# Kernel optimization log

Measured on AMD Instinct MI355X. Metric: run time of the kernel, lower is better.

The kernel has to match this reference:

```python
import jax, jax.numpy as jnp
import numpy as np

S, B, I = 512, 64, 1024
H = 1024 // 2  # per-direction hidden (MyBiGRU halves hidden_size)


def _gru(x, h0, Wx, Wh, b):
    """Single-direction GRU, faithful to MyGRU.forward.
    x: (S,B,I); h0: (B,H); Wx: (3,I,H) gates [r,u,h]; Wh: (3,H,H); b: (3,H).
    Note: candidate uses (reset_gate * state) @ Whh, matching torch operator
    precedence in `reset_gate * state @ self.weight_hh`.
    """
    # Precompute all input projections once: (S, 3, B, H)
    xg = jnp.einsum('sbi,gih->sgbh', x, Wx)

    def step(h, xt):
        r = jax.nn.sigmoid(xt[0] + h @ Wh[0] + b[0])
        u = jax.nn.sigmoid(xt[1] + h @ Wh[1] + b[1])
        c = jnp.tanh(xt[2] + (r * h) @ Wh[2] + b[2])
        h_new = u * h + (1.0 - u) * c
        return h_new, h_new

    h_last, hs = jax.lax.scan(step, h0, xg)
    return hs, h_last  # (S,B,H), (B,H)


def setup_inputs() -> dict:
    key = jax.random.key(0)
    ks = jax.random.split(key, 6)
    std = jnp.float32(0.01)
    return {
        "x": jax.random.normal(ks[0], (S, B, I), jnp.float32),
        "initial_state": jax.random.normal(ks[1], (B, 2 * H), jnp.float32),
        "Wx_f": std * jax.random.normal(ks[2], (3, I, H), jnp.float32),
        "Wh_f": std * jax.random.normal(ks[3], (3, H, H), jnp.float32),
        "b_f": jnp.zeros((3, H), jnp.float32),
        "Wx_b": std * jax.random.normal(ks[4], (3, I, H), jnp.float32),
        "Wh_b": std * jax.random.normal(ks[5], (3, H, H), jnp.float32),
        "b_b": jnp.zeros((3, H), jnp.float32),
    }


def reference(x, initial_state, Wx_f, Wh_f, b_f, Wx_b, Wh_b, b_b):
    h0_f = initial_state[:, :H]
    h0_b = initial_state[:, H:]
    fwd_out, fwd_state = _gru(x, h0_f, Wx_f, Wh_f, b_f)
    bwd_out, bwd_state = _gru(x[::-1], h0_b, Wx_b, Wh_b, b_b)
    outputs = jnp.concatenate([fwd_out, bwd_out[::-1]], axis=-1)  # (S,B,2H)
    state = jnp.concatenate([fwd_state, bwd_state], axis=-1)      # (B,2H)
    return outputs, state
```

## Files before the change

kernel.cpp:

```cpp
#include <hip/hip_runtime.h>
#include <hip/hip_bf16.h>


typedef __attribute__((ext_vector_type(8))) short short8;
typedef __attribute__((ext_vector_type(4))) float f32x4;

#define SENT 0x7FC0
#define SENT64 0x7FC07FC07FC07FC0ULL

__device__ __forceinline__ unsigned short f2bf(float f) {
    unsigned u = __builtin_bit_cast(unsigned, f);
    u += 0x7FFFu + ((u >> 16) & 1u);
    return (unsigned short)(u >> 16);
}
__device__ __forceinline__ float bf2f(unsigned short h) {
    unsigned u = ((unsigned)h) << 16;
    return __builtin_bit_cast(float, u);
}
__device__ __forceinline__ float xv(unsigned long long p, int jj) {
    return bf2f((unsigned short)(p >> (16 * jj)));
}
__device__ __forceinline__ int imin(int a, int b) { return a < b ? a : b; }


__global__ __launch_bounds__(256) void k_cvt_x(const float* __restrict__ x,
                                               unsigned short* __restrict__ xb) {
    size_t gid = (size_t)blockIdx.x * 256 + threadIdx.x;
    f32x4 a = ((const f32x4*)x)[gid * 2];
    f32x4 b = ((const f32x4*)x)[gid * 2 + 1];
    short8 o;
    o[0] = (short)f2bf(a[0]); o[1] = (short)f2bf(a[1]);
    o[2] = (short)f2bf(a[2]); o[3] = (short)f2bf(a[3]);
    o[4] = (short)f2bf(b[0]); o[5] = (short)f2bf(b[1]);
    o[6] = (short)f2bf(b[2]); o[7] = (short)f2bf(b[3]);
    ((short8*)xb)[gid] = o;
}

__global__ __launch_bounds__(256) void k_cvt_w(const float* __restrict__ Wxf,
                                               const float* __restrict__ Wxb,
                                               unsigned short* __restrict__ wt) {
    int gid = blockIdx.x * 256 + threadIdx.x;
    int n = gid >> 7, kc = gid & 127;
    const float* src = (n < 1536) ? Wxf : Wxb;
    int nn = (n >= 1536) ? n - 1536 : n;
    int g = nn >> 9, h = nn & 511;
    short8 o;
#pragma unroll
    for (int j = 0; j < 8; ++j)
        o[j] = (short)f2bf(src[(size_t)(g * 1024 + kc * 8 + j) * 512 + h]);
    *(short8*)(wt + (size_t)n * 1024 + kc * 8) = o;
}

__global__ __launch_bounds__(256) void k_cvt_whsl(const float* __restrict__ Whf,
                                                  const float* __restrict__ Whb,
                                                  unsigned short* __restrict__ o) {
    int gid = blockIdx.x * 256 + threadIdx.x;
    int kc = gid & 63;
    int r = gid >> 6;
    int c = r & 15; r >>= 4;
    int g = r % 3;  r /= 3;
    int w = r & 31, d = r >> 5;
    const float* src = d ? Whb : Whf;
    short8 v;
#pragma unroll
    for (int j = 0; j < 8; ++j)
        v[j] = (short)f2bf(src[(size_t)(g * 512 + kc * 8 + j) * 512 + w * 16 + c]);
    *(short8*)(o + ((size_t)((d * 32 + w) * 3 + g) * 16 + c) * 512 + kc * 8) = v;
}

__global__ __launch_bounds__(256) void k_sent(unsigned short* __restrict__ h4,
                                              unsigned short* __restrict__ rh4) {
    int gid = blockIdx.x * 256 + threadIdx.x;
    short8 s;
#pragma unroll
    for (int j = 0; j < 8; ++j) s[j] = (short)SENT;
    ((short8*)h4)[gid] = s;
    ((short8*)rh4)[gid] = s;
}

__global__ __launch_bounds__(256) void k_init(const float* __restrict__ h0,
                                              unsigned short* __restrict__ h4) {
    int gid = blockIdx.x * 256 + threadIdx.x;
    int b = gid >> 10, ch = gid & 1023;
    int d = ch >> 9, k = ch & 511;
    h4[((size_t)d * 64 + b) * 512 + k] = f2bf(h0[gid]);
}


__global__ __launch_bounds__(256) void k_gemm(const unsigned short* __restrict__ A,
                                              const unsigned short* __restrict__ Bt,
                                              unsigned short* __restrict__ C) {
    __shared__ unsigned short Al[128 * 40];
    __shared__ unsigned short Bl[128 * 40];
    const int n0 = blockIdx.x * 128;
    const int m0 = blockIdx.y * 128;
    const int t = threadIdx.x, wave = t >> 6, lane = t & 63;
    const int lg = lane >> 4, lr = lane & 15;
    const int wm = wave >> 1, wn = wave & 1;
    const int lrow = t >> 2, lkb = t & 3;

    f32x4 acc[4][4] = {};
    for (int kt = 0; kt < 32; ++kt) {
        const int k0 = kt * 32;
#pragma unroll
        for (int p = 0; p < 2; ++p) {
            int row = lrow + p * 64;
            *(short8*)(Al + row * 40 + lkb * 8) =
                *(const short8*)(A + (size_t)(m0 + row) * 1024 + k0 + lkb * 8);
            *(short8*)(Bl + row * 40 + lkb * 8) =
                *(const short8*)(Bt + (size_t)(n0 + row) * 1024 + k0 + lkb * 8);
        }
        __syncthreads();
        short8 af[4], bfr[4];
#pragma unroll
        for (int mi = 0; mi < 4; ++mi)
            af[mi] = *(const short8*)(Al + (wm * 64 + mi * 16 + lr) * 40 + lg * 8);
#pragma unroll
        for (int ni = 0; ni < 4; ++ni)
            bfr[ni] = *(const short8*)(Bl + (wn * 64 + ni * 16 + lr) * 40 + lg * 8);
#pragma unroll
        for (int mi = 0; mi < 4; ++mi)
#pragma unroll
            for (int ni = 0; ni < 4; ++ni)
                acc[mi][ni] = __builtin_amdgcn_mfma_f32_16x16x32_bf16(af[mi], bfr[ni],
                                                                      acc[mi][ni], 0, 0, 0);
        __syncthreads();
    }
#pragma unroll
    for (int mi = 0; mi < 4; ++mi)
#pragma unroll
        for (int ni = 0; ni < 4; ++ni) {
            int m = m0 + wm * 64 + mi * 16 + lg * 4;
            int n = n0 + wn * 64 + ni * 16 + lr;
            int dd = n >= 1536;
            int nn = n - dd * 1536;
            int g = nn >> 9, h = nn & 511;
            size_t colbase = (size_t)dd * 98304 + (size_t)(h >> 4) * 3072 +
                             (size_t)((h >> 2) & 3) * 12 + g * 4 + (h & 3);
#pragma unroll
            for (int jj = 0; jj < 4; ++jj) {
                int mm = m + jj;
                int s = mm >> 6, brow = mm & 63;
                C[(size_t)s * 196608 + colbase + (size_t)brow * 48] = f2bf(acc[mi][ni][jj]);
            }
        }
}


__device__ __forceinline__ void wait_frag(const char* p, short8* fr) {
    for (;;) {
        asm volatile(
            "global_load_dwordx4 %0, %16, off sc1\n\t"
            "global_load_dwordx4 %1, %16, off offset:64 sc1\n\t"
            "global_load_dwordx4 %2, %16, off offset:128 sc1\n\t"
            "global_load_dwordx4 %3, %16, off offset:192 sc1\n\t"
            "global_load_dwordx4 %4, %16, off offset:256 sc1\n\t"
            "global_load_dwordx4 %5, %16, off offset:320 sc1\n\t"
            "global_load_dwordx4 %6, %16, off offset:384 sc1\n\t"
            "global_load_dwordx4 %7, %16, off offset:448 sc1\n\t"
            "global_load_dwordx4 %8, %16, off offset:512 sc1\n\t"
            "global_load_dwordx4 %9, %16, off offset:576 sc1\n\t"
            "global_load_dwordx4 %10, %16, off offset:640 sc1\n\t"
            "global_load_dwordx4 %11, %16, off offset:704 sc1\n\t"
            "global_load_dwordx4 %12, %16, off offset:768 sc1\n\t"
            "global_load_dwordx4 %13, %16, off offset:832 sc1\n\t"
            "global_load_dwordx4 %14, %16, off offset:896 sc1\n\t"
            "global_load_dwordx4 %15, %16, off offset:960 sc1"
            : "=v"(fr[0]), "=v"(fr[1]), "=v"(fr[2]), "=v"(fr[3]),
              "=v"(fr[4]), "=v"(fr[5]), "=v"(fr[6]), "=v"(fr[7]),
              "=v"(fr[8]), "=v"(fr[9]), "=v"(fr[10]), "=v"(fr[11]),
              "=v"(fr[12]), "=v"(fr[13]), "=v"(fr[14]), "=v"(fr[15])
            : "v"(p) : "memory");
        asm volatile("s_waitcnt vmcnt(0)" ::: "memory");
        int bad = 0;
#pragma unroll
        for (int i = 0; i < 16; ++i)
            bad |= (((unsigned short)fr[i][0]) == SENT) |
                   (((unsigned short)fr[i][4]) == SENT);
        if (!__any(bad)) break;
        __builtin_amdgcn_s_sleep(2);
    }
    __builtin_amdgcn_sched_barrier(0);
}


__global__ __launch_bounds__(320) void k_rec(const unsigned short* __restrict__ xgr,
                                             const unsigned short* __restrict__ whsl,
                                             const float* __restrict__ h0,
                                             const float* __restrict__ b_f,
                                             const float* __restrict__ b_b,
                                             unsigned long long* h4,
                                             unsigned long long* rh4,
                                             float* __restrict__ out) {
    __shared__ char Wlb[98304];
    __shared__ char xls[24576];
    __shared__ int xg_ready;
    __shared__ int xg_ack[4];

    const int w = blockIdx.x;
    const int t = threadIdx.x;
    const int wave5 = t >> 6, lane = t & 63;

    if (t == 0) {
        xg_ready = 0;
        xg_ack[0] = xg_ack[1] = xg_ack[2] = xg_ack[3] = 0;
    }
    for (int i = 0; i < 20; ++i) {
        int c = t + i * 320;
        if (c < 6144) {
            int half = (c >= 3072);
            int byte = (c - half * 3072) << 4;
            int swz = byte ^ (((byte >> 10) & 7) << 4);
            *(short8*)(Wlb + half * 49152 + swz) =
                *(const short8*)((const char*)whsl + (size_t)(half * 32 + w) * 49152 + byte);
        }
    }
    __syncthreads();

    if (wave5 == 4) {
        for (int it = 0; it < 512; ++it) {
            if (it >= 2) {
                for (;;) {
                    int a0 = __hip_atomic_load(&xg_ack[0], __ATOMIC_RELAXED, __HIP_MEMORY_SCOPE_WORKGROUP);
                    int a1 = __hip_atomic_load(&xg_ack[1], __ATOMIC_RELAXED, __HIP_MEMORY_SCOPE_WORKGROUP);
                    int a2 = __hip_atomic_load(&xg_ack[2], __ATOMIC_RELAXED, __HIP_MEMORY_SCOPE_WORKGROUP);
                    int a3 = __hip_atomic_load(&xg_ack[3], __ATOMIC_RELAXED, __HIP_MEMORY_SCOPE_WORKGROUP);
                    if (imin(imin(a0, a1), imin(a2, a3)) >= it - 1) break;
                    __builtin_amdgcn_s_sleep(1);
                }
            }
            const char* pf = (const char*)xgr + (size_t)it * 393216 +
                             (size_t)w * 6144 + lane * 96;
            const char* pb = (const char*)xgr + (size_t)(511 - it) * 393216 + 196608 +
                             (size_t)w * 6144 + lane * 96;
            short8 vf[6], vb[6];
#pragma unroll
            for (int k = 0; k < 6; ++k) {
                vf[k] = *(const short8*)(pf + k * 16);
                vb[k] = *(const short8*)(pb + k * 16);
            }
            char* dst = xls + (it & 1) * 12288 + lane * 96;
#pragma unroll
            for (int k = 0; k < 6; ++k) {
                *(short8*)(dst + k * 16) = vf[k];
                *(short8*)(dst + 6144 + k * 16) = vb[k];
            }
            __builtin_amdgcn_fence(__ATOMIC_RELEASE, "workgroup");
            if (lane == 0)
                __hip_atomic_store(&xg_ready, it + 1, __ATOMIC_RELAXED, __HIP_MEMORY_SCOPE_WORKGROUP);
        }
        return;
    }

    const int wave = wave5, lg = lane >> 4, lr = lane & 15;
    const int b = wave * 16 + lr;
    const int cc = w * 16 + lg * 4;
    const int cswz = (lr & 7) << 4;

    const f32x4 bRf = *(const f32x4*)(b_f + cc);
    const f32x4 bUf = *(const f32x4*)(b_f + 512 + cc);
    const f32x4 bCf = *(const f32x4*)(b_f + 1024 + cc);
    const f32x4 bRb = *(const f32x4*)(b_b + cc);
    const f32x4 bUb = *(const f32x4*)(b_b + 512 + cc);
    const f32x4 bCb = *(const f32x4*)(b_b + 1024 + cc);

    float hf[4], hbo[4];
#pragma unroll
    for (int jj = 0; jj < 4; ++jj) {
        hf[jj]  = h0[(size_t)b * 1024 + cc + jj];
        hbo[jj] = h0[(size_t)b * 1024 + 512 + cc + jj];
    }

    const size_t rof = (size_t)b * 1024;
    const size_t rob = (size_t)(64 + b) * 1024;
    const int fro  = lg * 16;
    const int pubo = w * 32 + lg * 8;
    const int xoff = (b * 4 + lg) * 24;
    char* hbP = (char*)h4;
    char* rbP = (char*)rh4;

    for (int it = 0; it < 512; ++it) {
        const size_t slot  = (size_t)(it & 3) << 17;
        const size_t nslot = (size_t)((it + 1) & 3) << 17;
        const size_t oslot = (size_t)((it + 3) & 3) << 17;

        short8 fr[16];
        wait_frag(hbP + slot + rof + fro, fr);
        __hip_atomic_store((unsigned long long*)(hbP + oslot + rof + pubo), SENT64,
                           __ATOMIC_RELAXED, __HIP_MEMORY_SCOPE_AGENT);

        while (__hip_atomic_load(&xg_ready, __ATOMIC_RELAXED, __HIP_MEMORY_SCOPE_WORKGROUP) < it + 1)
            __builtin_amdgcn_s_sleep(1);
        __builtin_amdgcn_fence(__ATOMIC_ACQUIRE, "workgroup");
        const char* xp = xls + (it & 1) * 12288 + xoff;
        const unsigned long long xfR = *(const unsigned long long*)(xp);
        const unsigned long long xfU = *(const unsigned long long*)(xp + 8);
        const unsigned long long xfC = *(const unsigned long long*)(xp + 16);
        const unsigned long long xbR = *(const unsigned long long*)(xp + 6144);
        const unsigned long long xbU = *(const unsigned long long*)(xp + 6144 + 8);
        const unsigned long long xbC = *(const unsigned long long*)(xp + 6144 + 16);

        f32x4 aR = {0.f, 0.f, 0.f, 0.f}, aU = {0.f, 0.f, 0.f, 0.f};
#pragma unroll
        for (int ks = 0; ks < 16; ++ks) {
            int koff = ks * 64 + lg * 16;
            short8 w0 = *(const short8*)(Wlb + (((lr << 10) + koff) ^ cswz));
            short8 w1 = *(const short8*)(Wlb + ((16384 + (lr << 10) + koff) ^ cswz));
            aR = __builtin_amdgcn_mfma_f32_16x16x32_bf16(w0, fr[ks], aR, 0, 0, 0);
            aU = __builtin_amdgcn_mfma_f32_16x16x32_bf16(w1, fr[ks], aU, 0, 0, 0);
        }
        float uf[4];
        {
            unsigned long long rhp = 0;
#pragma unroll
            for (int jj = 0; jj < 4; ++jj) {
                float pr = aR[jj] + xv(xfR, jj) + bRf[jj];
                float pu = aU[jj] + xv(xfU, jj) + bUf[jj];
                float r = 1.f / (1.f + __expf(-pr));
                uf[jj] = 1.f / (1.f + __expf(-pu));
                rhp |= (unsigned long long)f2bf(r * hf[jj]) << (16 * jj);
            }
            __hip_atomic_store((unsigned long long*)(rbP + slot + rof + pubo), rhp,
                               __ATOMIC_RELAXED, __HIP_MEMORY_SCOPE_AGENT);
        }

        short8 fb[16];
        wait_frag(hbP + slot + rob + fro, fb);
        __hip_atomic_store((unsigned long long*)(hbP + oslot + rob + pubo), SENT64,
                           __ATOMIC_RELAXED, __HIP_MEMORY_SCOPE_AGENT);

        f32x4 cR = {0.f, 0.f, 0.f, 0.f}, cU = {0.f, 0.f, 0.f, 0.f};
#pragma unroll
        for (int ks = 0; ks < 16; ++ks) {
            int koff = ks * 64 + lg * 16;
            short8 w0 = *(const short8*)(Wlb + 49152 + (((lr << 10) + koff) ^ cswz));
            short8 w1 = *(const short8*)(Wlb + 49152 + ((16384 + (lr << 10) + koff) ^ cswz));
            cR = __builtin_amdgcn_mfma_f32_16x16x32_bf16(w0, fb[ks], cR, 0, 0, 0);
            cU = __builtin_amdgcn_mfma_f32_16x16x32_bf16(w1, fb[ks], cU, 0, 0, 0);
        }
        float ub[4];
        {
            unsigned long long rhp = 0;
#pragma unroll
            for (int jj = 0; jj < 4; ++jj) {
                float pr = cR[jj] + xv(xbR, jj) + bRb[jj];
                float pu = cU[jj] + xv(xbU, jj) + bUb[jj];
                float r = 1.f / (1.f + __expf(-pr));
                ub[jj] = 1.f / (1.f + __expf(-pu));
                rhp |= (unsigned long long)f2bf(r * hbo[jj]) << (16 * jj);
            }
            __hip_atomic_store((unsigned long long*)(rbP + slot + rob + pubo), rhp,
                               __ATOMIC_RELAXED, __HIP_MEMORY_SCOPE_AGENT);
        }

        short8 gr[16];
        wait_frag(rbP + slot + rof + fro, gr);
        __hip_atomic_store((unsigned long long*)(rbP + oslot + rof + pubo), SENT64,
                           __ATOMIC_RELAXED, __HIP_MEMORY_SCOPE_AGENT);

        f32x4 aC = {0.f, 0.f, 0.f, 0.f};
#pragma unroll
        for (int ks = 0; ks < 16; ++ks) {
            int koff = ks * 64 + lg * 16;
            short8 w2 = *(const short8*)(Wlb + ((32768 + (lr << 10) + koff) ^ cswz));
            aC = __builtin_amdgcn_mfma_f32_16x16x32_bf16(w2, gr[ks], aC, 0, 0, 0);
        }
        {
            f32x4 ov;
            unsigned long long hp = 0;
#pragma unroll
            for (int jj = 0; jj < 4; ++jj) {
                float pc = aC[jj] + xv(xfC, jj) + bCf[jj];
                float e = __expf(-2.f * pc);
                float c = 2.f / (1.f + e) - 1.f;
                float hn = uf[jj] * hf[jj] + (1.f - uf[jj]) * c;
                hf[jj] = hn;
                ov[jj] = hn;
                hp |= (unsigned long long)f2bf(hn) << (16 * jj);
            }
            __hip_atomic_store((unsigned long long*)(hbP + nslot + rof + pubo), hp,
                               __ATOMIC_RELAXED, __HIP_MEMORY_SCOPE_AGENT);
            *(f32x4*)(out + ((size_t)it * 64 + b) * 1024 + cc) = ov;
        }

        short8 gb[16];
        wait_frag(rbP + slot + rob + fro, gb);
        __hip_atomic_store((unsigned long long*)(rbP + oslot + rob + pubo), SENT64,
                           __ATOMIC_RELAXED, __HIP_MEMORY_SCOPE_AGENT);

        f32x4 cC = {0.f, 0.f, 0.f, 0.f};
#pragma unroll
        for (int ks = 0; ks < 16; ++ks) {
            int koff = ks * 64 + lg * 16;
            short8 w2 = *(const short8*)(Wlb + 49152 + ((32768 + (lr << 10) + koff) ^ cswz));
            cC = __builtin_amdgcn_mfma_f32_16x16x32_bf16(w2, gb[ks], cC, 0, 0, 0);
        }
        {
            f32x4 ov;
            unsigned long long hp = 0;
#pragma unroll
            for (int jj = 0; jj < 4; ++jj) {
                float pc = cC[jj] + xv(xbC, jj) + bCb[jj];
                float e = __expf(-2.f * pc);
                float c = 2.f / (1.f + e) - 1.f;
                float hn = ub[jj] * hbo[jj] + (1.f - ub[jj]) * c;
                hbo[jj] = hn;
                ov[jj] = hn;
                hp |= (unsigned long long)f2bf(hn) << (16 * jj);
            }
            __hip_atomic_store((unsigned long long*)(hbP + nslot + rob + pubo), hp,
                               __ATOMIC_RELAXED, __HIP_MEMORY_SCOPE_AGENT);
            *(f32x4*)(out + ((size_t)(511 - it) * 64 + b) * 1024 + 512 + cc) = ov;
        }

        if (lane == 0)
            __hip_atomic_store(&xg_ack[wave], it + 1, __ATOMIC_RELAXED, __HIP_MEMORY_SCOPE_WORKGROUP);
    }

    {
        f32x4 of = {hf[0], hf[1], hf[2], hf[3]};
        f32x4 ob = {hbo[0], hbo[1], hbo[2], hbo[3]};
        *(f32x4*)(out + (size_t)33554432 + (size_t)b * 1024 + cc) = of;
        *(f32x4*)(out + (size_t)33554432 + (size_t)b * 1024 + 512 + cc) = ob;
    }
}


extern "C" void kernel_launch(void* const* d_in, const int* in_sizes, int n_in,
                              void* d_out, int out_size, void* d_ws, size_t ws_size,
                              hipStream_t stream) {
    const float* x   = (const float*)d_in[0];
    const float* h0  = (const float*)d_in[1];
    const float* Wxf = (const float*)d_in[2];
    const float* Whf = (const float*)d_in[3];
    const float* bf_ = (const float*)d_in[4];
    const float* Wxb = (const float*)d_in[5];
    const float* Whb = (const float*)d_in[6];
    const float* bb_ = (const float*)d_in[7];
    float* out = (float*)d_out;

    char* ws = (char*)d_ws;
    size_t off = 0;
    auto take = [&](size_t bytes) {
        char* p = ws + off;
        off += (bytes + 255) & ~(size_t)255;
        return p;
    };
    unsigned short* xb   = (unsigned short*)take((size_t)33554432 * 2);
    unsigned short* wt   = (unsigned short*)take((size_t)3072 * 1024 * 2);
    unsigned short* xgr  = (unsigned short*)take((size_t)512 * 196608 * 2);
    unsigned short* whsl = (unsigned short*)take((size_t)2 * 32 * 3 * 16 * 512 * 2);
    unsigned long long* h4  = (unsigned long long*)take((size_t)4 * 131072);
    unsigned long long* rh4 = (unsigned long long*)take((size_t)4 * 131072);

    if (off > ws_size) return;

    hipLaunchKernelGGL(k_cvt_x,    dim3(16384),   dim3(256), 0, stream, x, xb);
    hipLaunchKernelGGL(k_cvt_w,    dim3(1536),    dim3(256), 0, stream, Wxf, Wxb, wt);
    hipLaunchKernelGGL(k_cvt_whsl, dim3(768),     dim3(256), 0, stream, Whf, Whb, whsl);
    hipLaunchKernelGGL(k_sent,     dim3(128),     dim3(256), 0, stream,
                       (unsigned short*)h4, (unsigned short*)rh4);
    hipLaunchKernelGGL(k_init,     dim3(256),     dim3(256), 0, stream, h0,
                       (unsigned short*)h4);
    hipLaunchKernelGGL(k_gemm,     dim3(24, 256), dim3(256), 0, stream, xb, wt, xgr);
    hipLaunchKernelGGL(k_rec,      dim3(32),      dim3(320), 0, stream, xgr, whsl, h0,
                       bf_, bb_, h4, rh4, out);
}
```

Before: 4.901 ms.

## Add per-wave progress counters to gate polling of recurrent state fragments

```diff
diff --git a/kernel.cpp b/kernel.cpp
--- a/kernel.cpp
+++ b/kernel.cpp
@@ -4,6 +4,7 @@
 
 typedef __attribute__((ext_vector_type(8))) short short8;
 typedef __attribute__((ext_vector_type(4))) float f32x4;
+typedef __attribute__((ext_vector_type(4))) int i32x4;
 
 #define SENT 0x7FC0
 #define SENT64 0x7FC07FC07FC07FC0ULL
@@ -21,6 +22,10 @@
     return bf2f((unsigned short)(p >> (16 * jj)));
 }
 __device__ __forceinline__ int imin(int a, int b) { return a < b ? a : b; }
+
+__device__ __forceinline__ void st_u16c(void* p, unsigned v) {
+    asm volatile("global_store_short %0, %1, off sc1" :: "v"(p), "v"(v) : "memory");
+}
 
 
 __global__ __launch_bounds__(256) void k_cvt_x(const float* __restrict__ x,
@@ -79,11 +84,13 @@
 }
 
 __global__ __launch_bounds__(256) void k_init(const float* __restrict__ h0,
-                                              unsigned short* __restrict__ h4) {
+                                              unsigned short* __restrict__ h4,
+                                              int* __restrict__ hint) {
     int gid = blockIdx.x * 256 + threadIdx.x;
     int b = gid >> 10, ch = gid & 1023;
     int d = ch >> 9, k = ch & 511;
     h4[((size_t)d * 64 + b) * 512 + k] = f2bf(h0[gid]);
+    if (gid < 256) hint[gid] = 0;
 }
 
 
@@ -144,6 +151,29 @@
                 C[(size_t)s * 196608 + colbase + (size_t)brow * 48] = f2bf(acc[mi][ni][jj]);
             }
         }
+}
+
+
+__device__ __forceinline__ void wait_hint(const char* p, int target) {
+    for (;;) {
+        i32x4 a, b, c, d;
+        asm volatile("global_load_dwordx4 %0, %4, off sc1\n\t"
+                     "global_load_dwordx4 %1, %4, off offset:16 sc1\n\t"
+                     "global_load_dwordx4 %2, %4, off offset:32 sc1\n\t"
+                     "global_load_dwordx4 %3, %4, off offset:48 sc1\n\t"
+                     "s_waitcnt vmcnt(0)"
+                     : "=v"(a), "=v"(b), "=v"(c), "=v"(d) : "v"(p) : "memory");
+        int ok = 1;
+#pragma unroll
+        for (int i = 0; i < 4; ++i) {
+            ok &= ((a[i] & 0xFFFF) >= target) & (((a[i] >> 16) & 0xFFFF) >= target);
+            ok &= ((b[i] & 0xFFFF) >= target) & (((b[i] >> 16) & 0xFFFF) >= target);
+            ok &= ((c[i] & 0xFFFF) >= target) & (((c[i] >> 16) & 0xFFFF) >= target);
+            ok &= ((d[i] & 0xFFFF) >= target) & (((d[i] >> 16) & 0xFFFF) >= target);
+        }
+        if (ok) break;
+        __builtin_amdgcn_s_sleep(1);
+    }
 }
 
 
@@ -191,6 +221,7 @@
                                              const float* __restrict__ b_b,
                                              unsigned long long* h4,
                                              unsigned long long* rh4,
+                                             int* hint,
                                              float* __restrict__ out) {
     __shared__ char Wlb[98304];
     __shared__ char xls[24576];
@@ -236,8 +267,8 @@
             short8 vf[6], vb[6];
 #pragma unroll
             for (int k = 0; k < 6; ++k) {
-                vf[k] = *(const short8*)(pf + k * 16);
-                vb[k] = *(const short8*)(pb + k * 16);
+                vf[k] = __builtin_nontemporal_load((const short8*)(pf + k * 16));
+                vb[k] = __builtin_nontemporal_load((const short8*)(pb + k * 16));
             }
             char* dst = xls + (it & 1) * 12288 + lane * 96;
 #pragma unroll
@@ -278,6 +309,11 @@
     const int xoff = (b * 4 + lg) * 24;
     char* hbP = (char*)h4;
     char* rbP = (char*)rh4;
+    char* hintB = (char*)hint;
+    char* ln_hf = hintB + (0 * 4 + wave) * 64;
+    char* ln_rf = hintB + (1 * 4 + wave) * 64;
+    char* ln_hb = hintB + (2 * 4 + wave) * 64;
+    char* ln_rb = hintB + (3 * 4 + wave) * 64;
 
     for (int it = 0; it < 512; ++it) {
         const size_t slot  = (size_t)(it & 3) << 17;
@@ -285,6 +321,7 @@
         const size_t oslot = (size_t)((it + 3) & 3) << 17;
 
         short8 fr[16];
+        wait_hint(ln_hf, it);
         wait_frag(hbP + slot + rof + fro, fr);
         __hip_atomic_store((unsigned long long*)(hbP + oslot + rof + pubo), SENT64,
                            __ATOMIC_RELAXED, __HIP_MEMORY_SCOPE_AGENT);
@@ -322,9 +359,12 @@
             }
             __hip_atomic_store((unsigned long long*)(rbP + slot + rof + pubo), rhp,
                                __ATOMIC_RELAXED, __HIP_MEMORY_SCOPE_AGENT);
+            asm volatile("s_waitcnt vmcnt(0)" ::: "memory");
+            if (lane == 0) st_u16c(ln_rf + w * 2, (unsigned)(it + 1));
         }
 
         short8 fb[16];
+        wait_hint(ln_hb, it);
         wait_frag(hbP + slot + rob + fro, fb);
         __hip_atomic_store((unsigned long long*)(hbP + oslot + rob + pubo), SENT64,
                            __ATOMIC_RELAXED, __HIP_MEMORY_SCOPE_AGENT);
@@ -351,9 +391,12 @@
             }
             __hip_atomic_store((unsigned long long*)(rbP + slot + rob + pubo), rhp,
                                __ATOMIC_RELAXED, __HIP_MEMORY_SCOPE_AGENT);
+            asm volatile("s_waitcnt vmcnt(0)" ::: "memory");
+            if (lane == 0) st_u16c(ln_rb + w * 2, (unsigned)(it + 1));
         }
 
         short8 gr[16];
+        wait_hint(ln_rf, it + 1);
         wait_frag(rbP + slot + rof + fro, gr);
         __hip_atomic_store((unsigned long long*)(rbP + oslot + rof + pubo), SENT64,
                            __ATOMIC_RELAXED, __HIP_MEMORY_SCOPE_AGENT);
@@ -380,10 +423,13 @@
             }
             __hip_atomic_store((unsigned long long*)(hbP + nslot + rof + pubo), hp,
                                __ATOMIC_RELAXED, __HIP_MEMORY_SCOPE_AGENT);
-            *(f32x4*)(out + ((size_t)it * 64 + b) * 1024 + cc) = ov;
+            asm volatile("s_waitcnt vmcnt(0)" ::: "memory");
+            if (lane == 0) st_u16c(ln_hf + w * 2, (unsigned)(it + 1));
+            __builtin_nontemporal_store(ov, (f32x4*)(out + ((size_t)it * 64 + b) * 1024 + cc));
         }
 
         short8 gb[16];
+        wait_hint(ln_rb, it + 1);
         wait_frag(rbP + slot + rob + fro, gb);
         __hip_atomic_store((unsigned long long*)(rbP + oslot + rob + pubo), SENT64,
                            __ATOMIC_RELAXED, __HIP_MEMORY_SCOPE_AGENT);
@@ -410,7 +456,10 @@
             }
             __hip_atomic_store((unsigned long long*)(hbP + nslot + rob + pubo), hp,
                                __ATOMIC_RELAXED, __HIP_MEMORY_SCOPE_AGENT);
-            *(f32x4*)(out + ((size_t)(511 - it) * 64 + b) * 1024 + 512 + cc) = ov;
+            asm volatile("s_waitcnt vmcnt(0)" ::: "memory");
+            if (lane == 0) st_u16c(ln_hb + w * 2, (unsigned)(it + 1));
+            __builtin_nontemporal_store(
+                ov, (f32x4*)(out + ((size_t)(511 - it) * 64 + b) * 1024 + 512 + cc));
         }
 
         if (lane == 0)
@@ -420,8 +469,8 @@
     {
         f32x4 of = {hf[0], hf[1], hf[2], hf[3]};
         f32x4 ob = {hbo[0], hbo[1], hbo[2], hbo[3]};
-        *(f32x4*)(out + (size_t)33554432 + (size_t)b * 1024 + cc) = of;
-        *(f32x4*)(out + (size_t)33554432 + (size_t)b * 1024 + 512 + cc) = ob;
+        __builtin_nontemporal_store(of, (f32x4*)(out + (size_t)33554432 + (size_t)b * 1024 + cc));
+        __builtin_nontemporal_store(ob, (f32x4*)(out + (size_t)33554432 + (size_t)b * 1024 + 512 + cc));
     }
 }
 
@@ -452,6 +501,7 @@
     unsigned short* whsl = (unsigned short*)take((size_t)2 * 32 * 3 * 16 * 512 * 2);
     unsigned long long* h4  = (unsigned long long*)take((size_t)4 * 131072);
     unsigned long long* rh4 = (unsigned long long*)take((size_t)4 * 131072);
+    int* hint            = (int*)take((size_t)1024);
 
     if (off > ws_size) return;
 
@@ -461,8 +511,8 @@
     hipLaunchKernelGGL(k_sent,     dim3(128),     dim3(256), 0, stream,
                        (unsigned short*)h4, (unsigned short*)rh4);
     hipLaunchKernelGGL(k_init,     dim3(256),     dim3(256), 0, stream, h0,
-                       (unsigned short*)h4);
+                       (unsigned short*)h4, hint);
     hipLaunchKernelGGL(k_gemm,     dim3(24, 256), dim3(256), 0, stream, xb, wt, xgr);
     hipLaunchKernelGGL(k_rec,      dim3(32),      dim3(320), 0, stream, xgr, whsl, h0,
-                       bf_, bb_, h4, rh4, out);
-}
+                       bf_, bb_, h4, rh4, hint, out);
+}
```

After: 7.082 ms. 44.5% more time.

## Halve recurrent compute waves, each handling two batch groups with merged fwd/bwd waits

Applied to the files above, without the earlier changes.

```diff
diff --git a/kernel.cpp b/kernel.cpp
--- a/kernel.cpp
+++ b/kernel.cpp
@@ -147,36 +147,44 @@
 }
 
 
-__device__ __forceinline__ void wait_frag(const char* p, short8* fr) {
+__device__ __forceinline__ void load16(const char* p, short8* fr) {
+    asm volatile(
+        "global_load_dwordx4 %0, %16, off sc1\n\t"
+        "global_load_dwordx4 %1, %16, off offset:64 sc1\n\t"
+        "global_load_dwordx4 %2, %16, off offset:128 sc1\n\t"
+        "global_load_dwordx4 %3, %16, off offset:192 sc1\n\t"
+        "global_load_dwordx4 %4, %16, off offset:256 sc1\n\t"
+        "global_load_dwordx4 %5, %16, off offset:320 sc1\n\t"
+        "global_load_dwordx4 %6, %16, off offset:384 sc1\n\t"
+        "global_load_dwordx4 %7, %16, off offset:448 sc1\n\t"
+        "global_load_dwordx4 %8, %16, off offset:512 sc1\n\t"
+        "global_load_dwordx4 %9, %16, off offset:576 sc1\n\t"
+        "global_load_dwordx4 %10, %16, off offset:640 sc1\n\t"
+        "global_load_dwordx4 %11, %16, off offset:704 sc1\n\t"
+        "global_load_dwordx4 %12, %16, off offset:768 sc1\n\t"
+        "global_load_dwordx4 %13, %16, off offset:832 sc1\n\t"
+        "global_load_dwordx4 %14, %16, off offset:896 sc1\n\t"
+        "global_load_dwordx4 %15, %16, off offset:960 sc1"
+        : "=v"(fr[0]), "=v"(fr[1]), "=v"(fr[2]), "=v"(fr[3]),
+          "=v"(fr[4]), "=v"(fr[5]), "=v"(fr[6]), "=v"(fr[7]),
+          "=v"(fr[8]), "=v"(fr[9]), "=v"(fr[10]), "=v"(fr[11]),
+          "=v"(fr[12]), "=v"(fr[13]), "=v"(fr[14]), "=v"(fr[15])
+        : "v"(p) : "memory");
+}
+
+__device__ __forceinline__ void wait2(const char* pf, const char* pb,
+                                      short8* fr, short8* fb) {
     for (;;) {
-        asm volatile(
-            "global_load_dwordx4 %0, %16, off sc1\n\t"
-            "global_load_dwordx4 %1, %16, off offset:64 sc1\n\t"
-            "global_load_dwordx4 %2, %16, off offset:128 sc1\n\t"
-            "global_load_dwordx4 %3, %16, off offset:192 sc1\n\t"
-            "global_load_dwordx4 %4, %16, off offset:256 sc1\n\t"
-            "global_load_dwordx4 %5, %16, off offset:320 sc1\n\t"
-            "global_load_dwordx4 %6, %16, off offset:384 sc1\n\t"
-            "global_load_dwordx4 %7, %16, off offset:448 sc1\n\t"
-            "global_load_dwordx4 %8, %16, off offset:512 sc1\n\t"
-            "global_load_dwordx4 %9, %16, off offset:576 sc1\n\t"
-            "global_load_dwordx4 %10, %16, off offset:640 sc1\n\t"
-            "global_load_dwordx4 %11, %16, off offset:704 sc1\n\t"
-            "global_load_dwordx4 %12, %16, off offset:768 sc1\n\t"
-            "global_load_dwordx4 %13, %16, off offset:832 sc1\n\t"
-            "global_load_dwordx4 %14, %16, off offset:896 sc1\n\t"
-            "global_load_dwordx4 %15, %16, off offset:960 sc1"
-            : "=v"(fr[0]), "=v"(fr[1]), "=v"(fr[2]), "=v"(fr[3]),
-              "=v"(fr[4]), "=v"(fr[5]), "=v"(fr[6]), "=v"(fr[7]),
-              "=v"(fr[8]), "=v"(fr[9]), "=v"(fr[10]), "=v"(fr[11]),
-              "=v"(fr[12]), "=v"(fr[13]), "=v"(fr[14]), "=v"(fr[15])
-            : "v"(p) : "memory");
+        load16(pf, fr);
+        load16(pb, fb);
         asm volatile("s_waitcnt vmcnt(0)" ::: "memory");
         int bad = 0;
 #pragma unroll
         for (int i = 0; i < 16; ++i)
             bad |= (((unsigned short)fr[i][0]) == SENT) |
-                   (((unsigned short)fr[i][4]) == SENT);
+                   (((unsigned short)fr[i][4]) == SENT) |
+                   (((unsigned short)fb[i][0]) == SENT) |
+                   (((unsigned short)fb[i][4]) == SENT);
         if (!__any(bad)) break;
         __builtin_amdgcn_s_sleep(2);
     }
@@ -184,48 +192,41 @@
 }
 
 
-__global__ __launch_bounds__(320) void k_rec(const unsigned short* __restrict__ xgr,
-                                             const unsigned short* __restrict__ whsl,
-                                             const float* __restrict__ h0,
-                                             const float* __restrict__ b_f,
-                                             const float* __restrict__ b_b,
-                                             unsigned long long* h4,
-                                             unsigned long long* rh4,
-                                             float* __restrict__ out) {
+__global__ __launch_bounds__(192, 1) void k_rec(const unsigned short* __restrict__ xgr,
+                                                const unsigned short* __restrict__ whsl,
+                                                const float* __restrict__ h0,
+                                                const float* __restrict__ b_f,
+                                                const float* __restrict__ b_b,
+                                                unsigned long long* h4,
+                                                unsigned long long* rh4,
+                                                float* __restrict__ out) {
     __shared__ char Wlb[98304];
     __shared__ char xls[24576];
     __shared__ int xg_ready;
-    __shared__ int xg_ack[4];
+    __shared__ int xg_ack[2];
 
     const int w = blockIdx.x;
     const int t = threadIdx.x;
-    const int wave5 = t >> 6, lane = t & 63;
-
-    if (t == 0) {
-        xg_ready = 0;
-        xg_ack[0] = xg_ack[1] = xg_ack[2] = xg_ack[3] = 0;
-    }
-    for (int i = 0; i < 20; ++i) {
-        int c = t + i * 320;
-        if (c < 6144) {
-            int half = (c >= 3072);
-            int byte = (c - half * 3072) << 4;
-            int swz = byte ^ (((byte >> 10) & 7) << 4);
-            *(short8*)(Wlb + half * 49152 + swz) =
-                *(const short8*)((const char*)whsl + (size_t)(half * 32 + w) * 49152 + byte);
-        }
+    const int wv = t >> 6, lane = t & 63;
+
+    if (t == 0) { xg_ready = 0; xg_ack[0] = xg_ack[1] = 0; }
+    for (int i = 0; i < 32; ++i) {
+        int c = t + i * 192;
+        int half = (c >= 3072);
+        int byte = (c - half * 3072) << 4;
+        int swz = byte ^ (((byte >> 10) & 7) << 4);
+        *(short8*)(Wlb + half * 49152 + swz) =
+            *(const short8*)((const char*)whsl + (size_t)(half * 32 + w) * 49152 + byte);
     }
     __syncthreads();
 
-    if (wave5 == 4) {
+    if (wv == 2) {
         for (int it = 0; it < 512; ++it) {
             if (it >= 2) {
                 for (;;) {
                     int a0 = __hip_atomic_load(&xg_ack[0], __ATOMIC_RELAXED, __HIP_MEMORY_SCOPE_WORKGROUP);
                     int a1 = __hip_atomic_load(&xg_ack[1], __ATOMIC_RELAXED, __HIP_MEMORY_SCOPE_WORKGROUP);
-                    int a2 = __hip_atomic_load(&xg_ack[2], __ATOMIC_RELAXED, __HIP_MEMORY_SCOPE_WORKGROUP);
-                    int a3 = __hip_atomic_load(&xg_ack[3], __ATOMIC_RELAXED, __HIP_MEMORY_SCOPE_WORKGROUP);
-                    if (imin(imin(a0, a1), imin(a2, a3)) >= it - 1) break;
+                    if (imin(a0, a1) >= it - 1) break;
                     __builtin_amdgcn_s_sleep(1);
                 }
             }
@@ -252,8 +253,7 @@
         return;
     }
 
-    const int wave = wave5, lg = lane >> 4, lr = lane & 15;
-    const int b = wave * 16 + lr;
+    const int lg = lane >> 4, lr = lane & 15;
     const int cc = w * 16 + lg * 4;
     const int cswz = (lr & 7) << 4;
 
@@ -264,164 +264,145 @@
     const f32x4 bUb = *(const f32x4*)(b_b + 512 + cc);
     const f32x4 bCb = *(const f32x4*)(b_b + 1024 + cc);
 
-    float hf[4], hbo[4];
-#pragma unroll
-    for (int jj = 0; jj < 4; ++jj) {
-        hf[jj]  = h0[(size_t)b * 1024 + cc + jj];
-        hbo[jj] = h0[(size_t)b * 1024 + 512 + cc + jj];
-    }
-
-    const size_t rof = (size_t)b * 1024;
-    const size_t rob = (size_t)(64 + b) * 1024;
+    int bg[2];
+    bg[0] = (wv * 2 + 0) * 16 + lr;
+    bg[1] = (wv * 2 + 1) * 16 + lr;
+
+    float hf[2][4], hbo[2][4];
+#pragma unroll
+    for (int g = 0; g < 2; ++g)
+#pragma unroll
+        for (int jj = 0; jj < 4; ++jj) {
+            hf[g][jj]  = h0[(size_t)bg[g] * 1024 + cc + jj];
+            hbo[g][jj] = h0[(size_t)bg[g] * 1024 + 512 + cc + jj];
+        }
+
+    size_t rof[2], rob[2];
+#pragma unroll
+    for (int g = 0; g < 2; ++g) {
+        rof[g] = (size_t)bg[g] * 1024;
+        rob[g] = (size_t)(64 + bg[g]) * 1024;
+    }
     const int fro  = lg * 16;
     const int pubo = w * 32 + lg * 8;
-    const int xoff = (b * 4 + lg) * 24;
     char* hbP = (char*)h4;
     char* rbP = (char*)rh4;
+
+    float uf[2][4], ub[2][4];
+    unsigned long long xfC[2], xbC[2];
 
     for (int it = 0; it < 512; ++it) {
         const size_t slot  = (size_t)(it & 3) << 17;
         const size_t nslot = (size_t)((it + 1) & 3) << 17;
         const size_t oslot = (size_t)((it + 3) & 3) << 17;
 
-        short8 fr[16];
-        wait_frag(hbP + slot + rof + fro, fr);
-        __hip_atomic_store((unsigned long long*)(hbP + oslot + rof + pubo), SENT64,
-                           __ATOMIC_RELAXED, __HIP_MEMORY_SCOPE_AGENT);
-
         while (__hip_atomic_load(&xg_ready, __ATOMIC_RELAXED, __HIP_MEMORY_SCOPE_WORKGROUP) < it + 1)
             __builtin_amdgcn_s_sleep(1);
         __builtin_amdgcn_fence(__ATOMIC_ACQUIRE, "workgroup");
-        const char* xp = xls + (it & 1) * 12288 + xoff;
-        const unsigned long long xfR = *(const unsigned long long*)(xp);
-        const unsigned long long xfU = *(const unsigned long long*)(xp + 8);
-        const unsigned long long xfC = *(const unsigned long long*)(xp + 16);
-        const unsigned long long xbR = *(const unsigned long long*)(xp + 6144);
-        const unsigned long long xbU = *(const unsigned long long*)(xp + 6144 + 8);
-        const unsigned long long xbC = *(const unsigned long long*)(xp + 6144 + 16);
-
-        f32x4 aR = {0.f, 0.f, 0.f, 0.f}, aU = {0.f, 0.f, 0.f, 0.f};
-#pragma unroll
-        for (int ks = 0; ks < 16; ++ks) {
-            int koff = ks * 64 + lg * 16;
-            short8 w0 = *(const short8*)(Wlb + (((lr << 10) + koff) ^ cswz));
-            short8 w1 = *(const short8*)(Wlb + ((16384 + (lr << 10) + koff) ^ cswz));
-            aR = __builtin_amdgcn_mfma_f32_16x16x32_bf16(w0, fr[ks], aR, 0, 0, 0);
-            aU = __builtin_amdgcn_mfma_f32_16x16x32_bf16(w1, fr[ks], aU, 0, 0, 0);
-        }
-        float uf[4];
-        {
-            unsigned long long rhp = 0;
+
+#pragma unroll
+        for (int g = 0; g < 2; ++g) {
+            short8 fr[16], fb[16];
+            wait2(hbP + slot + rof[g] + fro, hbP + slot + rob[g] + fro, fr, fb);
+            __hip_atomic_store((unsigned long long*)(hbP + oslot + rof[g] + pubo), SENT64,
+                               __ATOMIC_RELAXED, __HIP_MEMORY_SCOPE_AGENT);
+            __hip_atomic_store((unsigned long long*)(hbP + oslot + rob[g] + pubo), SENT64,
+                               __ATOMIC_RELAXED, __HIP_MEMORY_SCOPE_AGENT);
+
+            const char* xp = xls + (it & 1) * 12288 + (bg[g] * 4 + lg) * 24;
+            const unsigned long long xfR = *(const unsigned long long*)(xp);
+            const unsigned long long xfU = *(const unsigned long long*)(xp + 8);
+            xfC[g] = *(const unsigned long long*)(xp + 16);
+            const unsigned long long xbR = *(const unsigned long long*)(xp + 6144);
+            const unsigned long long xbU = *(const unsigned long long*)(xp + 6144 + 8);
+            xbC[g] = *(const unsigned long long*)(xp + 6144 + 16);
+
+            f32x4 aR = {0.f,0.f,0.f,0.f}, aU = {0.f,0.f,0.f,0.f};
+            f32x4 cR = {0.f,0.f,0.f,0.f}, cU = {0.f,0.f,0.f,0.f};
+#pragma unroll
+            for (int ks = 0; ks < 16; ++ks) {
+                int koff = ks * 64 + lg * 16;
+                short8 w0f = *(const short8*)(Wlb + (((lr << 10) + koff) ^ cswz));
+                short8 w1f = *(const short8*)(Wlb + ((16384 + (lr << 10) + koff) ^ cswz));
+                short8 w0b = *(const short8*)(Wlb + 49152 + (((lr << 10) + koff) ^ cswz));
+                short8 w1b = *(const short8*)(Wlb + 49152 + ((16384 + (lr << 10) + koff) ^ cswz));
+                aR = __builtin_amdgcn_mfma_f32_16x16x32_bf16(w0f, fr[ks], aR, 0, 0, 0);
+                aU = __builtin_amdgcn_mfma_f32_16x16x32_bf16(w1f, fr[ks], aU, 0, 0, 0);
+                cR = __builtin_amdgcn_mfma_f32_16x16x32_bf16(w0b, fb[ks], cR, 0, 0, 0);
+                cU = __builtin_amdgcn_mfma_f32_16x16x32_bf16(w1b, fb[ks], cU, 0, 0, 0);
+            }
+            unsigned long long rhpf = 0, rhpb = 0;
 #pragma unroll
             for (int jj = 0; jj < 4; ++jj) {
-                float pr = aR[jj] + xv(xfR, jj) + bRf[jj];
-                float pu = aU[jj] + xv(xfU, jj) + bUf[jj];
-                float r = 1.f / (1.f + __expf(-pr));
-                uf[jj] = 1.f / (1.f + __expf(-pu));
-                rhp |= (unsigned long long)f2bf(r * hf[jj]) << (16 * jj);
-            }
-            __hip_atomic_store((unsigned long long*)(rbP + slot + rof + pubo), rhp,
-                               __ATOMIC_RELAXED, __HIP_MEMORY_SCOPE_AGENT);
-        }
-
-        short8 fb[16];
-        wait_frag(hbP + slot + rob + fro, fb);
-        __hip_atomic_store((unsigned long long*)(hbP + oslot + rob + pubo), SENT64,
-                           __ATOMIC_RELAXED, __HIP_MEMORY_SCOPE_AGENT);
-
-        f32x4 cR = {0.f, 0.f, 0.f, 0.f}, cU = {0.f, 0.f, 0.f, 0.f};
-#pragma unroll
-        for (int ks = 0; ks < 16; ++ks) {
-            int koff = ks * 64 + lg * 16;
-            short8 w0 = *(const short8*)(Wlb + 49152 + (((lr << 10) + koff) ^ cswz));
-            short8 w1 = *(const short8*)(Wlb + 49152 + ((16384 + (lr << 10) + koff) ^ cswz));
-            cR = __builtin_amdgcn_mfma_f32_16x16x32_bf16(w0, fb[ks], cR, 0, 0, 0);
-            cU = __builtin_amdgcn_mfma_f32_16x16x32_bf16(w1, fb[ks], cU, 0, 0, 0);
-        }
-        float ub[4];
-        {
-            unsigned long long rhp = 0;
+                float prf = aR[jj] + xv(xfR, jj) + bRf[jj];
+                float puf = aU[jj] + xv(xfU, jj) + bUf[jj];
+                float prb = cR[jj] + xv(xbR, jj) + bRb[jj];
+                float pub_ = cU[jj] + xv(xbU, jj) + bUb[jj];
+                float rf_ = 1.f / (1.f + __expf(-prf));
+                float rb_ = 1.f / (1.f + __expf(-prb));
+                uf[g][jj] = 1.f / (1.f + __expf(-puf));
+                ub[g][jj] = 1.f / (1.f + __expf(-pub_));
+                rhpf |= (unsigned long long)f2bf(rf_ * hf[g][jj])  << (16 * jj);
+                rhpb |= (unsigned long long)f2bf(rb_ * hbo[g][jj]) << (16 * jj);
+            }
+            __hip_atomic_store((unsigned long long*)(rbP + slot + rof[g] + pubo), rhpf,
+                               __ATOMIC_RELAXED, __HIP_MEMORY_SCOPE_AGENT);
+            __hip_atomic_store((unsigned long long*)(rbP + slot + rob[g] + pubo), rhpb,
+                               __ATOMIC_RELAXED, __HIP_MEMORY_SCOPE_AGENT);
+        }
+
+#pragma unroll
+        for (int g = 0; g < 2; ++g) {
+            short8 gr[16], gb[16];
+            wait2(rbP + slot + rof[g] + fro, rbP + slot + rob[g] + fro, gr, gb);
+            __hip_atomic_store((unsigned long long*)(rbP + oslot + rof[g] + pubo), SENT64,
+                               __ATOMIC_RELAXED, __HIP_MEMORY_SCOPE_AGENT);
+            __hip_atomic_store((unsigned long long*)(rbP + oslot + rob[g] + pubo), SENT64,
+                               __ATOMIC_RELAXED, __HIP_MEMORY_SCOPE_AGENT);
+
+            f32x4 aC = {0.f,0.f,0.f,0.f}, cC = {0.f,0.f,0.f,0.f};
+#pragma unroll
+            for (int ks = 0; ks < 16; ++ks) {
+                int koff = ks * 64 + lg * 16;
+                short8 w2f = *(const short8*)(Wlb + ((32768 + (lr << 10) + koff) ^ cswz));
+                short8 w2b = *(const short8*)(Wlb + 49152 + ((32768 + (lr << 10) + koff) ^ cswz));
+                aC = __builtin_amdgcn_mfma_f32_16x16x32_bf16(w2f, gr[ks], aC, 0, 0, 0);
+                cC = __builtin_amdgcn_mfma_f32_16x16x32_bf16(w2b, gb[ks], cC, 0, 0, 0);
+            }
+            f32x4 ovf, ovb;
+            unsigned long long hpf = 0, hpb = 0;
 #pragma unroll
             for (int jj = 0; jj < 4; ++jj) {
-                float pr = cR[jj] + xv(xbR, jj) + bRb[jj];
-                float pu = cU[jj] + xv(xbU, jj) + bUb[jj];
-                float r = 1.f / (1.f + __expf(-pr));
-                ub[jj] = 1.f / (1.f + __expf(-pu));
-                rhp |= (unsigned long long)f2bf(r * hbo[jj]) << (16 * jj);
-            }
-            __hip_atomic_store((unsigned long long*)(rbP + slot + rob + pubo), rhp,
-                               __ATOMIC_RELAXED, __HIP_MEMORY_SCOPE_AGENT);
-        }
-
-        short8 gr[16];
-        wait_frag(rbP + slot + rof + fro, gr);
-        __hip_atomic_store((unsigned long long*)(rbP + oslot + rof + pubo), SENT64,
-                           __ATOMIC_RELAXED, __HIP_MEMORY_SCOPE_AGENT);
-
-        f32x4 aC = {0.f, 0.f, 0.f, 0.f};
-#pragma unroll
-        for (int ks = 0; ks < 16; ++ks) {
-            int koff = ks * 64 + lg * 16;
-            short8 w2 = *(const short8*)(Wlb + ((32768 + (lr << 10) + koff) ^ cswz));
-            aC = __builtin_amdgcn_mfma_f32_16x16x32_bf16(w2, gr[ks], aC, 0, 0, 0);
-        }
-        {
-            f32x4 ov;
-            unsigned long long hp = 0;
-#pragma unroll
-            for (int jj = 0; jj < 4; ++jj) {
-                float pc = aC[jj] + xv(xfC, jj) + bCf[jj];
-                float e = __expf(-2.f * pc);
-                float c = 2.f / (1.f + e) - 1.f;
-                float hn = uf[jj] * hf[jj] + (1.f - uf[jj]) * c;
-                hf[jj] = hn;
-                ov[jj] = hn;
-                hp |= (unsigned long long)f2bf(hn) << (16 * jj);
-            }
-            __hip_atomic_store((unsigned long long*)(hbP + nslot + rof + pubo), hp,
-                               __ATOMIC_RELAXED, __HIP_MEMORY_SCOPE_AGENT);
-            *(f32x4*)(out + ((size_t)it * 64 + b) * 1024 + cc) = ov;
-        }
-
-        short8 gb[16];
-        wait_frag(rbP + slot + rob + fro, gb);
-        __hip_atomic_store((unsigned long long*)(rbP + oslot + rob + pubo), SENT64,
-                           __ATOMIC_RELAXED, __HIP_MEMORY_SCOPE_AGENT);
-
-        f32x4 cC = {0.f, 0.f, 0.f, 0.f};
-#pragma unroll
-        for (int ks = 0; ks < 16; ++ks) {
-            int koff = ks * 64 + lg * 16;
-            short8 w2 = *(const short8*)(Wlb + 49152 + ((32768 + (lr << 10) + koff) ^ cswz));
-            cC = __builtin_amdgcn_mfma_f32_16x16x32_bf16(w2, gb[ks], cC, 0, 0, 0);
-        }
-        {
-            f32x4 ov;
-            unsigned long long hp = 0;
-#pragma unroll
-            for (int jj = 0; jj < 4; ++jj) {
-                float pc = cC[jj] + xv(xbC, jj) + bCb[jj];
-                float e = __expf(-2.f * pc);
-                float c = 2.f / (1.f + e) - 1.f;
-                float hn = ub[jj] * hbo[jj] + (1.f - ub[jj]) * c;
-                hbo[jj] = hn;
-                ov[jj] = hn;
-                hp |= (unsigned long long)f2bf(hn) << (16 * jj);
-            }
-            __hip_atomic_store((unsigned long long*)(hbP + nslot + rob + pubo), hp,
-                               __ATOMIC_RELAXED, __HIP_MEMORY_SCOPE_AGENT);
-            *(f32x4*)(out + ((size_t)(511 - it) * 64 + b) * 1024 + 512 + cc) = ov;
+                float pcf = aC[jj] + xv(xfC[g], jj) + bCf[jj];
+                float pcb = cC[jj] + xv(xbC[g], jj) + bCb[jj];
+                float ef = __expf(-2.f * pcf), eb = __expf(-2.f * pcb);
+                float cf = 2.f / (1.f + ef) - 1.f;
+                float cb = 2.f / (1.f + eb) - 1.f;
+                float hnf = uf[g][jj] * hf[g][jj]  + (1.f - uf[g][jj]) * cf;
+                float hnb = ub[g][jj] * hbo[g][jj] + (1.f - ub[g][jj]) * cb;
+                hf[g][jj] = hnf;  hbo[g][jj] = hnb;
+                ovf[jj] = hnf;    ovb[jj] = hnb;
+                hpf |= (unsigned long long)f2bf(hnf) << (16 * jj);
+                hpb |= (unsigned long long)f2bf(hnb) << (16 * jj);
+            }
+            __hip_atomic_store((unsigned long long*)(hbP + nslot + rof[g] + pubo), hpf,
+                               __ATOMIC_RELAXED, __HIP_MEMORY_SCOPE_AGENT);
+            __hip_atomic_store((unsigned long long*)(hbP + nslot + rob[g] + pubo), hpb,
+                               __ATOMIC_RELAXED, __HIP_MEMORY_SCOPE_AGENT);
+            *(f32x4*)(out + ((size_t)it * 64 + bg[g]) * 1024 + cc) = ovf;
+            *(f32x4*)(out + ((size_t)(511 - it) * 64 + bg[g]) * 1024 + 512 + cc) = ovb;
         }
 
         if (lane == 0)
-            __hip_atomic_store(&xg_ack[wave], it + 1, __ATOMIC_RELAXED, __HIP_MEMORY_SCOPE_WORKGROUP);
-    }
-
-    {
-        f32x4 of = {hf[0], hf[1], hf[2], hf[3]};
-        f32x4 ob = {hbo[0], hbo[1], hbo[2], hbo[3]};
-        *(f32x4*)(out + (size_t)33554432 + (size_t)b * 1024 + cc) = of;
-        *(f32x4*)(out + (size_t)33554432 + (size_t)b * 1024 + 512 + cc) = ob;
+            __hip_atomic_store(&xg_ack[wv], it + 1, __ATOMIC_RELAXED, __HIP_MEMORY_SCOPE_WORKGROUP);
+    }
+
+#pragma unroll
+    for (int g = 0; g < 2; ++g) {
+        f32x4 of = {hf[g][0], hf[g][1], hf[g][2], hf[g][3]};
+        f32x4 ob = {hbo[g][0], hbo[g][1], hbo[g][2], hbo[g][3]};
+        *(f32x4*)(out + (size_t)33554432 + (size_t)bg[g] * 1024 + cc) = of;
+        *(f32x4*)(out + (size_t)33554432 + (size_t)bg[g] * 1024 + 512 + cc) = ob;
     }
 }
 
@@ -463,6 +444,6 @@
     hipLaunchKernelGGL(k_init,     dim3(256),     dim3(256), 0, stream, h0,
                        (unsigned short*)h4);
     hipLaunchKernelGGL(k_gemm,     dim3(24, 256), dim3(256), 0, stream, xb, wt, xgr);
-    hipLaunchKernelGGL(k_rec,      dim3(32),      dim3(320), 0, stream, xgr, whsl, h0,
+    hipLaunchKernelGGL(k_rec,      dim3(32),      dim3(192), 0, stream, xgr, whsl, h0,
                        bf_, bb_, h4, rh4, out);
 }
```

Measured after the change: 7.271 ms. 1.48x slower.
